# Performance work log

Measured on AMD Instinct MI355X. Metric: run time of the kernel, lower is better.

Reference implementation:

```python
import jax, jax.numpy as jnp
import numpy as np

B, V, FIN, H = 200, 40, 16, 128
NSW = 12          # switch edges
NE = 40           # regular edges
M = NE + NSW      # 52 total edges
MLP_HID = 1024
OUT = M + V + NSW # 104


def _build_graph():
    rng = np.random.default_rng(0)
    pairs = set()
    while len(pairs) < M:
        i, j = map(int, rng.integers(0, V, 2))
        if i < j:
            pairs.add((i, j))
    pairs = sorted(pairs)
    reg = np.array(pairs[:NE], np.int64)   # (NE,2)
    sw = np.array(pairs[NE:], np.int64)    # (NSW,2) row-major sorted, matches torch.nonzero order
    edges = np.concatenate([reg, sw], 0)   # switch edges last, matching graph_topo layout
    A = np.zeros((V, M), np.float32)
    A[edges[:, 0], np.arange(M)] = 1.0
    A[edges[:, 1], np.arange(M)] = -1.0
    return reg, sw, A


def setup_inputs():
    key = jax.random.key(0)
    ks = jax.random.split(key, 16)
    reg, sw, A = _build_graph()
    ei = jnp.broadcast_to(jnp.asarray(reg.T)[None], (B, 2, NE))
    si = jnp.broadcast_to(jnp.asarray(sw.T)[None], (B, 2, NSW))

    def w(k, shp, fan):
        return jax.random.normal(k, shp, jnp.float32) / np.sqrt(fan)

    return {
        'x_mod': jax.random.normal(ks[0], (B, V, FIN), jnp.float32),
        'ei': ei, 'si': si, 'A_inc': jnp.asarray(A),
        'embed': w(ks[1], (2, FIN), 1.0),
        'WU0': w(ks[2], (FIN, H), FIN), 'WV0': w(ks[3], (FIN, H), FIN),
        'WA0': w(ks[4], (FIN, H), FIN), 'WB0': w(ks[5], (FIN, H), FIN),
        'WC0': w(ks[6], (FIN, H), FIN),
        'WU1': w(ks[7], (H, H), H), 'WV1': w(ks[8], (H, H), H),
        'WA1': w(ks[9], (H, H), H), 'WB1': w(ks[10], (H, H), H),
        'WC1': w(ks[11], (H, H), H),
        'W1': w(ks[12], ((NSW + V) * H, MLP_HID), (NSW + V) * H),
        'b1': jnp.zeros((MLP_HID,), jnp.float32),
        'W2': w(ks[13], (MLP_HID, OUT), MLP_HID),
        'b2': jnp.zeros((OUT,), jnp.float32),
    }


def _layer(x, s, adj, smask, WU, WV, WA, WB, WC, residual):
    Ux = x @ WU
    Vx = x @ WV
    # gate features over dense VxV switch grid: e_ij = A s_ij + B x_i + C x_j
    e = jnp.einsum('bijf,fh->bijh', s, WA) + (x @ WB)[:, :, None, :] + (x @ WC)[:, None, :, :]
    gates = jax.nn.sigmoid(e) * smask[..., None]
    msg_edges = jnp.einsum('bij,bjh->bih', adj, Vx)   # regular-edge aggregation
    msg_sw = jnp.einsum('bijh,bjh->bih', gates, Vx)   # gated switch aggregation
    xh = jax.nn.relu(Ux + msg_edges + msg_sw)
    sh = jax.nn.relu(e)
    if residual:
        xh = x + xh
        sh = s + sh
    return xh, sh


def reference(x_mod, ei, si, A_inc, embed, WU0, WV0, WA0, WB0, WC0,
              WU1, WV1, WA1, WB1, WC1, W1, b1, W2, b2):
    i_sw, j_sw = si[0, 0], si[0, 1]   # switch indices (shared across batch)
    i_e, j_e = ei[0, 0], ei[0, 1]
    S = jnp.zeros((V, V), bool).at[i_sw, j_sw].set(True)   # upper-tri switch mask
    smask = jnp.broadcast_to(S, (B, V, V)).astype(x_mod.dtype)
    s0 = embed[S.astype(jnp.int32)]                        # (V,V,FIN) edge embedding
    s = jnp.broadcast_to(s0[None], (B, V, V, FIN))
    adj1 = jnp.zeros((V, V), x_mod.dtype).at[i_e, j_e].set(1.0)
    adj = jnp.broadcast_to((adj1 + adj1.T)[None], (B, V, V))
    x, s = _layer(x_mod, s, adj, smask, WU0, WV0, WA0, WB0, WC0, residual=False)
    x, s = _layer(x, s, adj, smask, WU1, WV1, WA1, WB1, WC1, residual=True)
    switches = s[:, i_sw, j_sw, :]                         # (B,NSW,H) irregular gather (torch.nonzero path)
    mlp_in = jnp.concatenate([switches.reshape(B, -1), x.reshape(B, -1)], axis=1)
    out = jax.nn.relu(mlp_in @ W1 + b1) @ W2 + b2          # (B,OUT)
    p_switch = jax.nn.sigmoid(out[:, -NSW:])
    graph_topo = jnp.ones((B, M), out.dtype).at[:, M - NSW:].set(p_switch)
    v = out[:, M:M + V].at[:, 0].set(1.0)
    p_fc = graph_topo * out[:, :M]
    q_fc = graph_topo * (v @ A_inc)                        # per-edge voltage difference flow
    pg = x_mod[:, :, 0] + jnp.einsum('vm,bm->bv', A_inc, p_fc)  # power balance completion
    qg = x_mod[:, :, 1] + jnp.einsum('vm,bm->bv', A_inc, q_fc)
    z = jnp.concatenate([p_fc, v, graph_topo], axis=1)     # (B, 2M+V)
    zc = jnp.concatenate([q_fc, pg, qg], axis=1)           # (B, M+2V)
    return z, zc
```

## Files before the change

kernel.cpp:

```cpp
#include <hip/hip_runtime.h>
#include <math.h>

#define B       200
#define V       40
#define FIN     16
#define H       128
#define NSW     12
#define NE      40
#define M       52
#define MLP_HID 1024
#define OUTD    104
#define MLP_IN  6656
#define ZDIM    144
#define ZCDIM   132
#define NCH     13
#define X1LD    136
#define MAXD    16

typedef __attribute__((ext_vector_type(8))) short bf16x8;
typedef __attribute__((ext_vector_type(4))) float f32x4;

__device__ __forceinline__ float sigmoidf(float x) {
    return 1.0f / (1.0f + expf(-x));
}
__device__ __forceinline__ unsigned short f2b(float x) {
    unsigned int u = __float_as_uint(x);
    u += 0x7fffu + ((u >> 16) & 1u);
    return (unsigned short)(u >> 16);
}
__device__ __forceinline__ float b2f(unsigned short s) {
    return __uint_as_float(((unsigned int)s) << 16);
}

__global__ __launch_bounds__(256) void k_prep(
        const float* __restrict__ WU0, const float* __restrict__ WV0,
        const float* __restrict__ WB0, const float* __restrict__ WC0,
        const float* __restrict__ WU1, const float* __restrict__ WV1,
        const float* __restrict__ WB1, const float* __restrict__ WC1,
        const float* __restrict__ WA1, const float* __restrict__ W2,
        unsigned short* __restrict__ W0t, unsigned short* __restrict__ Wt640,
        unsigned short* __restrict__ W2t) {
    int bx = blockIdx.x, tid = threadIdx.x;
    if (bx < 64) {
        int o0 = bx * 2048 + tid * 8;
#pragma unroll
        for (int i = 0; i < 8; ++i) {
            int o = o0 + i; int col = o >> 10, k = o & 1023;
            W2t[o] = (col < OUTD) ? f2b(W2[(size_t)k * OUTD + col]) : (unsigned short)0;
        }
    } else if (bx < 104) {
        int o0 = (bx - 64) * 2048 + tid * 8;
#pragma unroll
        for (int i = 0; i < 8; ++i) {
            int o = o0 + i; int col = o >> 7, f = o & 127;
            int m = col >> 7, hh = col & 127;
            const float* Ws = (m == 0) ? WU1 : (m == 1) ? WV1 : (m == 2) ? WB1
                            : (m == 3) ? WC1 : WA1;
            Wt640[o] = f2b(Ws[f * H + hh]);
        }
    } else {
        int o0 = (bx - 104) * 2048 + tid * 8;
#pragma unroll
        for (int i = 0; i < 8; ++i) {
            int o = o0 + i; int col = o >> 5, k = o & 31;
            int m = col >> 7, hh = col & 127;
            const float* Ws = (m == 0) ? WU0 : (m == 1) ? WV0 : (m == 2) ? WB0 : WC0;
            W0t[o] = (k < FIN) ? f2b(Ws[k * H + hh]) : (unsigned short)0;
        }
    }
}

__global__ __launch_bounds__(512) void k_gnn(const float* __restrict__ x,
        const int* __restrict__ ei, const int* __restrict__ si,
        const float* __restrict__ embed, const float* __restrict__ WA0,
        const unsigned short* __restrict__ W0t,
        const unsigned short* __restrict__ Wt640,
        unsigned short* __restrict__ Abf) {
    int b = blockIdx.x, tid = threadIdx.x;
    __shared__ unsigned short xb[48 * 40];
    __shared__ unsigned short uvbc[V * 512];
    __shared__ unsigned short x1l[64 * X1LD];
    __shared__ float gL[NSW * H];
    __shared__ float sA1l[NSW * H];
    __shared__ int   nbr[V][MAXD];
    __shared__ int   deg[V];

    int h = tid & 127, sub = tid >> 7;
    int lane = tid & 63, wv = tid >> 6;
    int lr = lane & 15, lk = lane >> 4;
    int n0w = wv * 64;

    for (int o = tid; o < 48 * 32; o += 512) {
        int r = o >> 5, k = o & 31;
        float v = (r < V && k < FIN) ? x[(size_t)b * V * FIN + r * FIN + k] : 0.f;
        xb[r * 40 + k] = f2b(v);
    }
    if (tid < V) deg[tid] = 0;
    for (int o = tid; o < 12 * 128; o += 512) {
        int rr = o >> 7;
        int row = (rr < 8) ? 40 + rr : 60 + (rr - 8);
        x1l[row * X1LD + (o & 127)] = 0;
    }
    __syncthreads();

    if (tid < NE) {
        int i = ei[tid], j = ei[NE + tid];
        int p = atomicAdd(&deg[i], 1); if (p < MAXD) nbr[i][p] = j;
        int q = atomicAdd(&deg[j], 1); if (q < MAXD) nbr[j][q] = i;
    } else if (tid < NE + NSW) {
        int k = tid - NE;
        int i = si[k], j = si[NSW + k];
        int p = atomicAdd(&deg[i], 1); if (p < MAXD) nbr[i][p] = j | ((k + 1) << 8);
    }
    {
        f32x4 acc[3][4];
#pragma unroll
        for (int rf = 0; rf < 3; ++rf)
#pragma unroll
            for (int cf = 0; cf < 4; ++cf) acc[rf][cf] = (f32x4){0.f, 0.f, 0.f, 0.f};
        int kseg = lk * 8;
        bf16x8 a0 = *(const bf16x8*)&xb[lr * 40 + kseg];
        bf16x8 a1 = *(const bf16x8*)&xb[(16 + lr) * 40 + kseg];
        bf16x8 a2 = *(const bf16x8*)&xb[(32 + lr) * 40 + kseg];
#pragma unroll
        for (int cf = 0; cf < 4; ++cf) {
            bf16x8 bf = *(const bf16x8*)&W0t[(n0w + cf * 16 + lr) * 32 + kseg];
            acc[0][cf] = __builtin_amdgcn_mfma_f32_16x16x32_bf16(a0, bf, acc[0][cf], 0, 0, 0);
            acc[1][cf] = __builtin_amdgcn_mfma_f32_16x16x32_bf16(a1, bf, acc[1][cf], 0, 0, 0);
            acc[2][cf] = __builtin_amdgcn_mfma_f32_16x16x32_bf16(a2, bf, acc[2][cf], 0, 0, 0);
        }
#pragma unroll
        for (int rf = 0; rf < 3; ++rf)
#pragma unroll
            for (int cf = 0; cf < 4; ++cf)
#pragma unroll
                for (int r = 0; r < 4; ++r) {
                    int row = rf * 16 + lk * 4 + r;
                    if (row < V) uvbc[row * 512 + n0w + cf * 16 + lr] = f2b(acc[rf][cf][r]);
                }
    }
    __syncthreads();

    {
        float sA0 = 0.f;
#pragma unroll
        for (int f = 0; f < FIN; ++f) sA0 += embed[FIN + f] * WA0[f * H + h];
        for (int k = sub; k < NSW; k += 4) {
            int i = si[k], j = si[NSW + k];
            float e0 = sA0 + b2f(uvbc[i * 512 + 256 + h]) + b2f(uvbc[j * 512 + 384 + h]);
            gL[k * H + h] = sigmoidf(e0);
            x1l[(48 + k) * X1LD + h] = f2b(fmaxf(e0, 0.f));
        }
    }
    __syncthreads();

    for (int i = sub * 10; i < sub * 10 + 10; ++i) {
        float acc = b2f(uvbc[i * 512 + h]);
        int d = deg[i]; if (d > MAXD) d = MAXD;
        for (int p = 0; p < d; ++p) {
            int ent = nbr[i][p];
            float vv = b2f(uvbc[(ent & 255) * 512 + 128 + h]);
            int g = ent >> 8;
            if (g) vv *= gL[(g - 1) * H + h];
            acc += vv;
        }
        x1l[i * X1LD + h] = f2b(fmaxf(acc, 0.f));
    }
    __syncthreads();

    {
        f32x4 acc[3][4], accs = (f32x4){0.f, 0.f, 0.f, 0.f};
#pragma unroll
        for (int rf = 0; rf < 3; ++rf)
#pragma unroll
            for (int cf = 0; cf < 4; ++cf) acc[rf][cf] = (f32x4){0.f, 0.f, 0.f, 0.f};
#pragma unroll
        for (int kk = 0; kk < 4; ++kk) {
            int kseg = kk * 32 + lk * 8;
            bf16x8 a0 = *(const bf16x8*)&x1l[lr * X1LD + kseg];
            bf16x8 a1 = *(const bf16x8*)&x1l[(16 + lr) * X1LD + kseg];
            bf16x8 a2 = *(const bf16x8*)&x1l[(32 + lr) * X1LD + kseg];
            bf16x8 as = *(const bf16x8*)&x1l[(48 + lr) * X1LD + kseg];
#pragma unroll
            for (int cf = 0; cf < 4; ++cf) {
                bf16x8 bf = *(const bf16x8*)&Wt640[(size_t)(n0w + cf * 16 + lr) * H + kseg];
                acc[0][cf] = __builtin_amdgcn_mfma_f32_16x16x32_bf16(a0, bf, acc[0][cf], 0, 0, 0);
                acc[1][cf] = __builtin_amdgcn_mfma_f32_16x16x32_bf16(a1, bf, acc[1][cf], 0, 0, 0);
                acc[2][cf] = __builtin_amdgcn_mfma_f32_16x16x32_bf16(a2, bf, acc[2][cf], 0, 0, 0);
            }
            bf16x8 bs = *(const bf16x8*)&Wt640[(size_t)(512 + wv * 16 + lr) * H + kseg];
            accs = __builtin_amdgcn_mfma_f32_16x16x32_bf16(as, bs, accs, 0, 0, 0);
        }
#pragma unroll
        for (int rf = 0; rf < 3; ++rf)
#pragma unroll
            for (int cf = 0; cf < 4; ++cf)
#pragma unroll
                for (int r = 0; r < 4; ++r) {
                    int row = rf * 16 + lk * 4 + r;
                    if (row < V) uvbc[row * 512 + n0w + cf * 16 + lr] = f2b(acc[rf][cf][r]);
                }
#pragma unroll
        for (int r = 0; r < 4; ++r) {
            int sr = lk * 4 + r;
            if (sr < NSW) sA1l[sr * H + wv * 16 + lr] = accs[r];
        }
    }
    __syncthreads();

    for (int k = sub; k < NSW; k += 4) {
        int i = si[k], j = si[NSW + k];
        float e1 = sA1l[k * H + h] + b2f(uvbc[i * 512 + 256 + h]) + b2f(uvbc[j * 512 + 384 + h]);
        gL[k * H + h] = sigmoidf(e1);
        float s1 = b2f(x1l[(48 + k) * X1LD + h]);
        Abf[(size_t)b * MLP_IN + k * H + h] = f2b(s1 + fmaxf(e1, 0.f));
    }
    __syncthreads();

    for (int i = sub * 10; i < sub * 10 + 10; ++i) {
        float acc = b2f(uvbc[i * 512 + h]);
        int d = deg[i]; if (d > MAXD) d = MAXD;
        for (int p = 0; p < d; ++p) {
            int ent = nbr[i][p];
            float vv = b2f(uvbc[(ent & 255) * 512 + 128 + h]);
            int g = ent >> 8;
            if (g) vv *= gL[(g - 1) * H + h];
            acc += vv;
        }
        float x2 = b2f(x1l[i * X1LD + h]) + fmaxf(acc, 0.f);
        Abf[(size_t)b * MLP_IN + NSW * H + i * H + h] = f2b(x2);
    }
}

__global__ __launch_bounds__(256) void k_mlp(const unsigned short* __restrict__ A,
        const float* __restrict__ W1, float* __restrict__ partial) {
    const int NK = 16;
    int tid = threadIdx.x;
    int lane = tid & 63, wvv = tid >> 6;
    int n0 = blockIdx.x * 64;
    int kbase = blockIdx.z * NK * 32;

    __shared__ __align__(16) unsigned short a_lds[256 * 40];
    __shared__ __align__(16) unsigned short b_lds[64 * 40];

    f32x4 acc[4][4];
#pragma unroll
    for (int rf = 0; rf < 4; ++rf)
#pragma unroll
        for (int cf = 0; cf < 4; ++cf) acc[rf][cf] = (f32x4){0.f, 0.f, 0.f, 0.f};

    int srow = tid >> 2, sseg = tid & 3;
    const unsigned short* gA = A + (size_t)srow * MLP_IN + kbase + sseg * 8;
    int lwsA = srow * 40 + sseg * 8;

    int bcol = tid & 63, bkg = tid >> 6;
    const float* gW = W1 + (size_t)(kbase + bkg * 8) * MLP_HID + n0 + bcol;
    int lwsB = bcol * 40 + bkg * 8;

    int lr = lane & 15, lk = lane >> 4;
    int a_off = (wvv * 64 + lr) * 40 + lk * 8;
    int b_off = lr * 40 + lk * 8;

    int4 ra[4];
    float rfv[8];
#pragma unroll
    for (int g = 0; g < 4; ++g)
        ra[g] = *(const int4*)(gA + (size_t)g * 64 * MLP_IN);
#pragma unroll
    for (int i = 0; i < 8; ++i) rfv[i] = gW[(size_t)i * MLP_HID];

    for (int kk = 0; kk < NK; ++kk) {
#pragma unroll
        for (int g = 0; g < 4; ++g)
            *(int4*)&a_lds[lwsA + g * 64 * 40] = ra[g];
        {
            union { unsigned short us[8]; int4 v; } pk;
#pragma unroll
            for (int i = 0; i < 8; ++i) pk.us[i] = f2b(rfv[i]);
            *(int4*)&b_lds[lwsB] = pk.v;
        }
        __syncthreads();
        if (kk + 1 < NK) {
#pragma unroll
            for (int g = 0; g < 4; ++g)
                ra[g] = *(const int4*)(gA + (size_t)g * 64 * MLP_IN + (kk + 1) * 32);
            const float* g2 = gW + (size_t)(kk + 1) * 32 * MLP_HID;
#pragma unroll
            for (int i = 0; i < 8; ++i) rfv[i] = g2[(size_t)i * MLP_HID];
        }
        bf16x8 af[4], bf[4];
#pragma unroll
        for (int rf = 0; rf < 4; ++rf) af[rf] = *(const bf16x8*)&a_lds[a_off + rf * 16 * 40];
#pragma unroll
        for (int cf = 0; cf < 4; ++cf) bf[cf] = *(const bf16x8*)&b_lds[b_off + cf * 16 * 40];
#pragma unroll
        for (int rf = 0; rf < 4; ++rf)
#pragma unroll
            for (int cf = 0; cf < 4; ++cf)
                acc[rf][cf] = __builtin_amdgcn_mfma_f32_16x16x32_bf16(af[rf], bf[cf], acc[rf][cf], 0, 0, 0);
        __syncthreads();
    }

    float* dst = partial + (size_t)blockIdx.z * 256 * MLP_HID;
#pragma unroll
    for (int rf = 0; rf < 4; ++rf)
#pragma unroll
        for (int cf = 0; cf < 4; ++cf) {
            int row = wvv * 64 + rf * 16 + lk * 4;
            int col = n0 + cf * 16 + lr;
#pragma unroll
            for (int e = 0; e < 4; ++e)
                dst[(size_t)(row + e) * MLP_HID + col] = acc[rf][cf][e];
        }
}

template<int MODE>
__global__ __launch_bounds__(256) void k_gemm(const unsigned short* __restrict__ A,
        const unsigned short* __restrict__ Bt, void* __restrict__ Cout,
        int K, int nk, int ldc) {
    int tid = threadIdx.x;
    int lane = tid & 63, wv = tid >> 6;
    int wr = (wv >> 1) * 32, wc = (wv & 1) * 32;
    int n0 = blockIdx.x * 64, m0 = blockIdx.y * 64;
    size_t kbase = (size_t)blockIdx.z * nk * 32;

    __shared__ __align__(16) unsigned short a_lds[64 * 40];
    __shared__ __align__(16) unsigned short b_lds[64 * 40];

    f32x4 acc00 = {0,0,0,0}, acc01 = {0,0,0,0}, acc10 = {0,0,0,0}, acc11 = {0,0,0,0};

    int srow = tid >> 2, sseg = tid & 3;
    const int4* gA = (const int4*)(A + (size_t)(m0 + srow) * K + kbase + sseg * 8);
    const int4* gB = (const int4*)(Bt + (size_t)(n0 + srow) * K + kbase + sseg * 8);
    int lws = srow * 40 + sseg * 8;

    int a_off = (wr + (lane & 15)) * 40 + (lane >> 4) * 8;
    int b_off = (wc + (lane & 15)) * 40 + (lane >> 4) * 8;

    int4 ra = gA[0], rb = gB[0];
    for (int kk = 0; kk < nk; ++kk) {
        *(int4*)&a_lds[lws] = ra;
        *(int4*)&b_lds[lws] = rb;
        __syncthreads();
        if (kk + 1 < nk) { ra = gA[(kk + 1) * 4]; rb = gB[(kk + 1) * 4]; }
        bf16x8 a0 = *(const bf16x8*)&a_lds[a_off];
        bf16x8 a1 = *(const bf16x8*)&a_lds[a_off + 16 * 40];
        bf16x8 b0 = *(const bf16x8*)&b_lds[b_off];
        bf16x8 b1 = *(const bf16x8*)&b_lds[b_off + 16 * 40];
        acc00 = __builtin_amdgcn_mfma_f32_16x16x32_bf16(a0, b0, acc00, 0, 0, 0);
        acc01 = __builtin_amdgcn_mfma_f32_16x16x32_bf16(a0, b1, acc01, 0, 0, 0);
        acc10 = __builtin_amdgcn_mfma_f32_16x16x32_bf16(a1, b0, acc10, 0, 0, 0);
        acc11 = __builtin_amdgcn_mfma_f32_16x16x32_bf16(a1, b1, acc11, 0, 0, 0);
        __syncthreads();
    }

    int crow = (lane >> 4) * 4, ccol = lane & 15;
    int row0 = m0 + wr + crow, row1 = row0 + 16;
    int col0 = n0 + wc + ccol, col1 = col0 + 16;
    float* dst = (float*)Cout + (size_t)blockIdx.z * (gridDim.y * 64) * ldc;
#pragma unroll
    for (int r = 0; r < 4; ++r) {
        dst[(size_t)(row0 + r) * ldc + col0] = acc00[r];
        dst[(size_t)(row0 + r) * ldc + col1] = acc01[r];
        dst[(size_t)(row1 + r) * ldc + col0] = acc10[r];
        dst[(size_t)(row1 + r) * ldc + col1] = acc11[r];
    }
}

__global__ void k_mred(const float* __restrict__ partial, const float* __restrict__ b1,
                       unsigned short* __restrict__ hiddenb) {
    int i = blockIdx.x * 256 + threadIdx.x;
    float s = b1[i & (MLP_HID - 1)];
#pragma unroll
    for (int z = 0; z < NCH; ++z) s += partial[(size_t)z * 256 * MLP_HID + i];
    hiddenb[i] = f2b(fmaxf(s, 0.f));
}

__global__ __launch_bounds__(128) void k_fin(const float* __restrict__ partial2,
        const float* __restrict__ b2, const float* __restrict__ A,
        const float* __restrict__ x_mod, float* __restrict__ outp) {
    int b = blockIdx.x;
    int tid = threadIdx.x;
    __shared__ float o[OUTD];
    __shared__ float gt[M], vv[V], pfc[M], qfc[M];

    if (tid < OUTD) {
        float s = b2[tid];
#pragma unroll
        for (int z = 0; z < 4; ++z) s += partial2[(size_t)z * 256 * 128 + b * 128 + tid];
        o[tid] = s;
    }
    __syncthreads();

    if (tid < M) {
        float g = (tid < M - NSW) ? 1.0f : sigmoidf(o[M + V + (tid - (M - NSW))]);
        gt[tid] = g;
        pfc[tid] = g * o[tid];
    }
    if (tid < V) vv[tid] = (tid == 0) ? 1.0f : o[M + tid];
    __syncthreads();

    if (tid < M) {
        float acc = 0.f;
        for (int x = 0; x < V; ++x) acc += vv[x] * A[x * M + tid];
        qfc[tid] = gt[tid] * acc;
    }
    __syncthreads();

    float* zb = outp + (size_t)b * ZDIM;
    if (tid < M) zb[tid] = pfc[tid];
    if (tid < V) zb[M + tid] = vv[tid];
    if (tid < M) zb[M + V + tid] = gt[tid];

    float* zcb = outp + (size_t)B * ZDIM + (size_t)b * ZCDIM;
    if (tid < M) zcb[tid] = qfc[tid];
    if (tid < V) {
        float accp = 0.f, accq = 0.f;
        for (int m = 0; m < M; ++m) {
            float a = A[tid * M + m];
            accp += a * pfc[m];
            accq += a * qfc[m];
        }
        zcb[M + tid]     = x_mod[(size_t)(b * V + tid) * FIN + 0] + accp;
        zcb[M + V + tid] = x_mod[(size_t)(b * V + tid) * FIN + 1] + accq;
    }
}

extern "C" void kernel_launch(void* const* d_in, const int* in_sizes, int n_in,
                              void* d_out, int out_size, void* d_ws, size_t ws_size,
                              hipStream_t stream) {
    const float* x_mod = (const float*)d_in[0];
    const int*   ei    = (const int*)d_in[1];
    const int*   si    = (const int*)d_in[2];
    const float* A     = (const float*)d_in[3];
    const float* embed = (const float*)d_in[4];
    const float* WU0   = (const float*)d_in[5];
    const float* WV0   = (const float*)d_in[6];
    const float* WA0   = (const float*)d_in[7];
    const float* WB0   = (const float*)d_in[8];
    const float* WC0   = (const float*)d_in[9];
    const float* WU1   = (const float*)d_in[10];
    const float* WV1   = (const float*)d_in[11];
    const float* WA1   = (const float*)d_in[12];
    const float* WB1   = (const float*)d_in[13];
    const float* WC1   = (const float*)d_in[14];
    const float* W1    = (const float*)d_in[15];
    const float* b1    = (const float*)d_in[16];
    const float* W2    = (const float*)d_in[17];
    const float* b2    = (const float*)d_in[18];
    float* out = (float*)d_out;

    char* ws = (char*)d_ws;
    unsigned short* W0t      = (unsigned short*)(ws + 0);
    unsigned short* Wt640    = (unsigned short*)(ws + 32768);
    unsigned short* W2t      = (unsigned short*)(ws + 196608);
    unsigned short* Abf      = (unsigned short*)(ws + 458752);
    float*          partialM = (float*)(ws + 3866624);
    unsigned short* hiddenb  = (unsigned short*)(ws + 17498112);
    float*          partial2 = (float*)(ws + 18022400);

    k_prep<<<112, 256, 0, stream>>>(WU0, WV0, WB0, WC0, WU1, WV1, WB1, WC1, WA1, W2,
                                    W0t, Wt640, W2t);
    k_gnn<<<B, 512, 0, stream>>>(x_mod, ei, si, embed, WA0, W0t, Wt640, Abf);
    k_mlp<<<dim3(16, 1, NCH), 256, 0, stream>>>(Abf, W1, partialM);
    k_mred<<<256 * MLP_HID / 256, 256, 0, stream>>>(partialM, b1, hiddenb);
    k_gemm<2><<<dim3(2, 4, 4), 256, 0, stream>>>(hiddenb, W2t, partial2, MLP_HID, 8, 128);
    k_fin<<<B, 128, 0, stream>>>(partial2, b2, A, x_mod, out);
}
```

Baseline: 67.94 us.

## Split MLP GEMM rows across two blocks and fuse hidden reduction into head GEMM

The first MLP GEMM now splits the 256 batch rows into two 128-row blocks, doubling the grid from 208 to 416 blocks. In exchange, each W1 tile is read and converted to bf16 twice. The separate split-K reduction kernel is removed. The second GEMM now sums the 13 partials, adds bias, applies ReLU and converts to bf16 while staging its A tile, which saves a launch and the hidden-buffer round trip. The risk is that each head block re-reads the partials redundantly across its 2 column blocks, on a small grid.

Result: faster. 65.56 us (-3.5%).

```diff
diff --git a/kernel.cpp b/kernel.cpp
--- a/kernel.cpp
+++ b/kernel.cpp
@@ -238,41 +238,41 @@
     int tid = threadIdx.x;
     int lane = tid & 63, wvv = tid >> 6;
     int n0 = blockIdx.x * 64;
+    int m0 = blockIdx.y * 128;
     int kbase = blockIdx.z * NK * 32;
 
-    __shared__ __align__(16) unsigned short a_lds[256 * 40];
+    __shared__ __align__(16) unsigned short a_lds[128 * 40];
     __shared__ __align__(16) unsigned short b_lds[64 * 40];
 
-    f32x4 acc[4][4];
-#pragma unroll
-    for (int rf = 0; rf < 4; ++rf)
+    f32x4 acc[2][4];
+#pragma unroll
+    for (int rf = 0; rf < 2; ++rf)
 #pragma unroll
         for (int cf = 0; cf < 4; ++cf) acc[rf][cf] = (f32x4){0.f, 0.f, 0.f, 0.f};
 
-    int srow = tid >> 2, sseg = tid & 3;
-    const unsigned short* gA = A + (size_t)srow * MLP_IN + kbase + sseg * 8;
-    int lwsA = srow * 40 + sseg * 8;
+    int sr0 = tid >> 2, ss = tid & 3;
+    const unsigned short* gA0 = A + (size_t)(m0 + sr0) * MLP_IN + kbase + ss * 8;
+    const unsigned short* gA1 = gA0 + (size_t)64 * MLP_IN;
+    int lwsA0 = sr0 * 40 + ss * 8;
+    int lwsA1 = (sr0 + 64) * 40 + ss * 8;
 
     int bcol = tid & 63, bkg = tid >> 6;
     const float* gW = W1 + (size_t)(kbase + bkg * 8) * MLP_HID + n0 + bcol;
     int lwsB = bcol * 40 + bkg * 8;
 
     int lr = lane & 15, lk = lane >> 4;
-    int a_off = (wvv * 64 + lr) * 40 + lk * 8;
+    int a_off = (wvv * 32 + lr) * 40 + lk * 8;
     int b_off = lr * 40 + lk * 8;
 
-    int4 ra[4];
+    int4 ra0 = *(const int4*)gA0;
+    int4 ra1 = *(const int4*)gA1;
     float rfv[8];
 #pragma unroll
-    for (int g = 0; g < 4; ++g)
-        ra[g] = *(const int4*)(gA + (size_t)g * 64 * MLP_IN);
-#pragma unroll
     for (int i = 0; i < 8; ++i) rfv[i] = gW[(size_t)i * MLP_HID];
 
     for (int kk = 0; kk < NK; ++kk) {
-#pragma unroll
-        for (int g = 0; g < 4; ++g)
-            *(int4*)&a_lds[lwsA + g * 64 * 40] = ra[g];
+        *(int4*)&a_lds[lwsA0] = ra0;
+        *(int4*)&a_lds[lwsA1] = ra1;
         {
             union { unsigned short us[8]; int4 v; } pk;
 #pragma unroll
@@ -281,32 +281,31 @@
         }
         __syncthreads();
         if (kk + 1 < NK) {
-#pragma unroll
-            for (int g = 0; g < 4; ++g)
-                ra[g] = *(const int4*)(gA + (size_t)g * 64 * MLP_IN + (kk + 1) * 32);
+            ra0 = *(const int4*)(gA0 + (kk + 1) * 32);
+            ra1 = *(const int4*)(gA1 + (kk + 1) * 32);
             const float* g2 = gW + (size_t)(kk + 1) * 32 * MLP_HID;
 #pragma unroll
             for (int i = 0; i < 8; ++i) rfv[i] = g2[(size_t)i * MLP_HID];
         }
-        bf16x8 af[4], bf[4];
-#pragma unroll
-        for (int rf = 0; rf < 4; ++rf) af[rf] = *(const bf16x8*)&a_lds[a_off + rf * 16 * 40];
-#pragma unroll
-        for (int cf = 0; cf < 4; ++cf) bf[cf] = *(const bf16x8*)&b_lds[b_off + cf * 16 * 40];
-#pragma unroll
-        for (int rf = 0; rf < 4; ++rf)
+        bf16x8 af[2], bfv[4];
+#pragma unroll
+        for (int rf = 0; rf < 2; ++rf) af[rf] = *(const bf16x8*)&a_lds[a_off + rf * 16 * 40];
+#pragma unroll
+        for (int cf = 0; cf < 4; ++cf) bfv[cf] = *(const bf16x8*)&b_lds[b_off + cf * 16 * 40];
+#pragma unroll
+        for (int rf = 0; rf < 2; ++rf)
 #pragma unroll
             for (int cf = 0; cf < 4; ++cf)
-                acc[rf][cf] = __builtin_amdgcn_mfma_f32_16x16x32_bf16(af[rf], bf[cf], acc[rf][cf], 0, 0, 0);
+                acc[rf][cf] = __builtin_amdgcn_mfma_f32_16x16x32_bf16(af[rf], bfv[cf], acc[rf][cf], 0, 0, 0);
         __syncthreads();
     }
 
     float* dst = partial + (size_t)blockIdx.z * 256 * MLP_HID;
 #pragma unroll
-    for (int rf = 0; rf < 4; ++rf)
+    for (int rf = 0; rf < 2; ++rf)
 #pragma unroll
         for (int cf = 0; cf < 4; ++cf) {
-            int row = wvv * 64 + rf * 16 + lk * 4;
+            int row = m0 + wvv * 32 + rf * 16 + lk * 4;
             int col = n0 + cf * 16 + lr;
 #pragma unroll
             for (int e = 0; e < 4; ++e)
@@ -314,15 +313,15 @@
         }
 }
 
-template<int MODE>
-__global__ __launch_bounds__(256) void k_gemm(const unsigned short* __restrict__ A,
-        const unsigned short* __restrict__ Bt, void* __restrict__ Cout,
-        int K, int nk, int ldc) {
+__global__ __launch_bounds__(256) void k_head(const float* __restrict__ partialM,
+        const float* __restrict__ b1, const unsigned short* __restrict__ W2t,
+        float* __restrict__ partial2) {
+    const int NK = 8;
     int tid = threadIdx.x;
     int lane = tid & 63, wv = tid >> 6;
     int wr = (wv >> 1) * 32, wc = (wv & 1) * 32;
     int n0 = blockIdx.x * 64, m0 = blockIdx.y * 64;
-    size_t kbase = (size_t)blockIdx.z * nk * 32;
+    int kbase = blockIdx.z * NK * 32;
 
     __shared__ __align__(16) unsigned short a_lds[64 * 40];
     __shared__ __align__(16) unsigned short b_lds[64 * 40];
@@ -330,50 +329,58 @@
     f32x4 acc00 = {0,0,0,0}, acc01 = {0,0,0,0}, acc10 = {0,0,0,0}, acc11 = {0,0,0,0};
 
     int srow = tid >> 2, sseg = tid & 3;
-    const int4* gA = (const int4*)(A + (size_t)(m0 + srow) * K + kbase + sseg * 8);
-    const int4* gB = (const int4*)(Bt + (size_t)(n0 + srow) * K + kbase + sseg * 8);
-    int lws = srow * 40 + sseg * 8;
+    const float* gH = partialM + (size_t)(m0 + srow) * MLP_HID + kbase + sseg * 8;
+    const float* gb = b1 + kbase + sseg * 8;
+    int lwsA = srow * 40 + sseg * 8;
+
+    const int4* gB = (const int4*)(W2t + (size_t)(n0 + srow) * MLP_HID + kbase + sseg * 8);
 
     int a_off = (wr + (lane & 15)) * 40 + (lane >> 4) * 8;
     int b_off = (wc + (lane & 15)) * 40 + (lane >> 4) * 8;
 
-    int4 ra = gA[0], rb = gB[0];
-    for (int kk = 0; kk < nk; ++kk) {
-        *(int4*)&a_lds[lws] = ra;
-        *(int4*)&b_lds[lws] = rb;
+    int4 rb = gB[0];
+    for (int kk = 0; kk < NK; ++kk) {
+        {
+            float s[8];
+#pragma unroll
+            for (int i = 0; i < 8; ++i) s[i] = gb[kk * 32 + i];
+#pragma unroll
+            for (int z = 0; z < NCH; ++z) {
+                const float4* p = (const float4*)(gH + (size_t)z * 256 * MLP_HID + kk * 32);
+                float4 v0 = p[0], v1 = p[1];
+                s[0] += v0.x; s[1] += v0.y; s[2] += v0.z; s[3] += v0.w;
+                s[4] += v1.x; s[5] += v1.y; s[6] += v1.z; s[7] += v1.w;
+            }
+            union { unsigned short us[8]; int4 v; } pa;
+#pragma unroll
+            for (int i = 0; i < 8; ++i) pa.us[i] = f2b(fmaxf(s[i], 0.f));
+            *(int4*)&a_lds[lwsA] = pa.v;
+        }
+        *(int4*)&b_lds[lwsA] = rb;
         __syncthreads();
-        if (kk + 1 < nk) { ra = gA[(kk + 1) * 4]; rb = gB[(kk + 1) * 4]; }
+        if (kk + 1 < NK) rb = gB[(kk + 1) * 4];
         bf16x8 a0 = *(const bf16x8*)&a_lds[a_off];
         bf16x8 a1 = *(const bf16x8*)&a_lds[a_off + 16 * 40];
         bf16x8 b0 = *(const bf16x8*)&b_lds[b_off];
-        bf16x8 b1 = *(const bf16x8*)&b_lds[b_off + 16 * 40];
+        bf16x8 b1v = *(const bf16x8*)&b_lds[b_off + 16 * 40];
         acc00 = __builtin_amdgcn_mfma_f32_16x16x32_bf16(a0, b0, acc00, 0, 0, 0);
-        acc01 = __builtin_amdgcn_mfma_f32_16x16x32_bf16(a0, b1, acc01, 0, 0, 0);
+        acc01 = __builtin_amdgcn_mfma_f32_16x16x32_bf16(a0, b1v, acc01, 0, 0, 0);
         acc10 = __builtin_amdgcn_mfma_f32_16x16x32_bf16(a1, b0, acc10, 0, 0, 0);
-        acc11 = __builtin_amdgcn_mfma_f32_16x16x32_bf16(a1, b1, acc11, 0, 0, 0);
+        acc11 = __builtin_amdgcn_mfma_f32_16x16x32_bf16(a1, b1v, acc11, 0, 0, 0);
         __syncthreads();
     }
 
     int crow = (lane >> 4) * 4, ccol = lane & 15;
     int row0 = m0 + wr + crow, row1 = row0 + 16;
     int col0 = n0 + wc + ccol, col1 = col0 + 16;
-    float* dst = (float*)Cout + (size_t)blockIdx.z * (gridDim.y * 64) * ldc;
+    float* dst = partial2 + (size_t)blockIdx.z * 256 * 128;
 #pragma unroll
     for (int r = 0; r < 4; ++r) {
-        dst[(size_t)(row0 + r) * ldc + col0] = acc00[r];
-        dst[(size_t)(row0 + r) * ldc + col1] = acc01[r];
-        dst[(size_t)(row1 + r) * ldc + col0] = acc10[r];
-        dst[(size_t)(row1 + r) * ldc + col1] = acc11[r];
-    }
-}
-
-__global__ void k_mred(const float* __restrict__ partial, const float* __restrict__ b1,
-                       unsigned short* __restrict__ hiddenb) {
-    int i = blockIdx.x * 256 + threadIdx.x;
-    float s = b1[i & (MLP_HID - 1)];
-#pragma unroll
-    for (int z = 0; z < NCH; ++z) s += partial[(size_t)z * 256 * MLP_HID + i];
-    hiddenb[i] = f2b(fmaxf(s, 0.f));
+        dst[(size_t)(row0 + r) * 128 + col0] = acc00[r];
+        dst[(size_t)(row0 + r) * 128 + col1] = acc01[r];
+        dst[(size_t)(row1 + r) * 128 + col0] = acc10[r];
+        dst[(size_t)(row1 + r) * 128 + col1] = acc11[r];
+    }
 }
 
 __global__ __launch_bounds__(128) void k_fin(const float* __restrict__ partial2,
@@ -456,14 +463,12 @@
     unsigned short* W2t      = (unsigned short*)(ws + 196608);
     unsigned short* Abf      = (unsigned short*)(ws + 458752);
     float*          partialM = (float*)(ws + 3866624);
-    unsigned short* hiddenb  = (unsigned short*)(ws + 17498112);
-    float*          partial2 = (float*)(ws + 18022400);
+    float*          partial2 = (float*)(ws + 17498112);
 
     k_prep<<<112, 256, 0, stream>>>(WU0, WV0, WB0, WC0, WU1, WV1, WB1, WC1, WA1, W2,
                                     W0t, Wt640, W2t);
     k_gnn<<<B, 512, 0, stream>>>(x_mod, ei, si, embed, WA0, W0t, Wt640, Abf);
-    k_mlp<<<dim3(16, 1, NCH), 256, 0, stream>>>(Abf, W1, partialM);
-    k_mred<<<256 * MLP_HID / 256, 256, 0, stream>>>(partialM, b1, hiddenb);
-    k_gemm<2><<<dim3(2, 4, 4), 256, 0, stream>>>(hiddenb, W2t, partial2, MLP_HID, 8, 128);
+    k_mlp<<<dim3(16, 2, NCH), 256, 0, stream>>>(Abf, W1, partialM);
+    k_head<<<dim3(2, 4, 4), 256, 0, stream>>>(partialM, b1, W2t, partial2);
     k_fin<<<B, 128, 0, stream>>>(partial2, b2, A, x_mod, out);
 }
```
